# Performance work log

Hardware: AMD Instinct MI355X
Metric: run time of the kernel (lower is better)

The kernel has to match this reference:

```python
import jax, jax.numpy as jnp
import numpy as np

N, E, G = 65536, 262144, 2048
DIN, H, F, L, P, TASK = 9, 300, 32, 5, 3, 1
DG = H + F + 1024 + 167  # 1523


def setup_inputs() -> dict:
    key = jax.random.key(0)
    ks = jax.random.split(key, 24)
    s = 0.02
    inp = {
        'x': jax.random.normal(ks[0], (N, DIN), jnp.float32),
        'morgan': jax.random.uniform(ks[1], (G, 1024), jnp.float32),
        'maccs': jax.random.uniform(ks[2], (G, 167), jnp.float32),
        'edge_index': jax.random.randint(ks[3], (2, E), 0, N, jnp.int32),
        'batch': jnp.sort(jax.random.randint(ks[4], (N,), 0, G, jnp.int32)),
        # node feature encoder
        'W_emb': s * jax.random.normal(ks[5], (DIN, H), jnp.float32),
        'b_emb': jnp.zeros((H,), jnp.float32),
        # GIN conv MLPs (L layers): H -> 2H -> H
        'gin_W1': s * jax.random.normal(ks[6], (L, H, 2 * H), jnp.float32),
        'gin_b1': jnp.zeros((L, 2 * H), jnp.float32),
        'gin_W2': s * jax.random.normal(ks[7], (L, 2 * H, H), jnp.float32),
        'gin_b2': jnp.zeros((L, H), jnp.float32),
        'bn_scale': jnp.ones((L, H), jnp.float32),
        'bn_bias': jnp.zeros((L, H), jnp.float32),
        'eps': jnp.zeros((L,), jnp.float32),
        # virtual node: init embedding + update MLPs (L-1 layers)
        'vn0': jnp.zeros((H,), jnp.float32),
        'vn_W1': s * jax.random.normal(ks[8], (L - 1, H, 2 * H), jnp.float32),
        'vn_b1': jnp.zeros((L - 1, 2 * H), jnp.float32),
        'vn_W2': s * jax.random.normal(ks[9], (L - 1, 2 * H, H), jnp.float32),
        'vn_b2': jnp.zeros((L - 1, H), jnp.float32),
        # predictor MLP: DG -> 2H -> TASK
        'Wp1': s * jax.random.normal(ks[10], (DG, 2 * H), jnp.float32),
        'bp1': jnp.zeros((2 * H,), jnp.float32),
        'Wp2': s * jax.random.normal(ks[11], (2 * H, TASK), jnp.float32),
        'bp2': jnp.zeros((TASK,), jnp.float32),
    }
    return inp


def _seg_mean(v, seg, n):
    s = jax.ops.segment_sum(v, seg, num_segments=n)
    c = jax.ops.segment_sum(jnp.ones((v.shape[0], 1), v.dtype), seg, num_segments=n)
    return s / jnp.maximum(c, 1.0)


def _bn(z, scale, bias):
    m = z.mean(0)
    v = z.var(0)
    return (z - m) * jax.lax.rsqrt(v + 1e-5) * scale + bias


def _gnn_and_predict(x, morgan, maccs, W_emb, b_emb, gin_W1, gin_b1, gin_W2, gin_b2,
                     bn_scale, bn_bias, eps, vn0, vn_W1, vn_b1, vn_W2, vn_b2,
                     Wp1, bp1, Wp2, bp2, edge_index, batch):
    n = x.shape[0]
    g = morgan.shape[0]
    nl = gin_W1.shape[0]
    src, dst = edge_index[0], edge_index[1]

    # GIN-virtual backbone (eval mode, dropout off). Note: GNN input is the
    # original x (the permuted ids are appended AFTER the GNN), so h is
    # permutation-independent and computed once.
    h = x @ W_emb + b_emb
    vn = jnp.broadcast_to(vn0, (g, vn0.shape[0]))
    for l in range(nl):
        hv = h + vn[batch]                                       # [N,H]
        agg = jax.ops.segment_sum(hv[src], dst, num_segments=n)  # neighbor sum
        z = (1.0 + eps[l]) * hv + agg
        z = jax.nn.relu(z @ gin_W1[l] + gin_b1[l]) @ gin_W2[l] + gin_b2[l]
        z = _bn(z, bn_scale[l], bn_bias[l])
        if l < nl - 1:
            z = jax.nn.relu(z)
        h = h + z  # residual
        if l < nl - 1:  # virtual node update
            vt = jax.ops.segment_sum(hv, batch, num_segments=g) + vn
            vn = vn + jax.nn.relu(jax.nn.relu(vt @ vn_W1[l] + vn_b1[l]) @ vn_W2[l] + vn_b2[l])

    pooled_h = _seg_mean(h, batch, g)  # [G,H]

    # Segmented random permutation of tiled eye(F) ids, averaged over P perms.
    # Each node gets one_hot(perm_rank_within_graph % F); rank computed by a
    # single lexsort over (batch, random) instead of a per-graph Python loop.
    counts = jax.ops.segment_sum(jnp.ones((n,), jnp.int32), batch, num_segments=g)
    starts = jnp.concatenate([jnp.zeros((1,), jnp.int32),
                              jnp.cumsum(counts)[:-1].astype(jnp.int32)])
    pkey = jax.random.key(42)
    acc = jnp.zeros((g, F), h.dtype)
    for p in range(P):
        r = jax.random.uniform(jax.random.fold_in(pkey, p), (n,))
        order = jnp.lexsort((r, batch))                       # sort by graph, then random
        local = jnp.arange(n, dtype=jnp.int32) - starts[batch[order]]
        rank = jnp.zeros((n,), jnp.int32).at[order].set(local)  # random rank in graph
        ids = jax.nn.one_hot(rank % F, F, dtype=h.dtype)        # [N,F]
        acc = acc + _seg_mean(ids, batch, g)
    id_pool = acc / P

    # h_rep order matches torch: [pooled h | pooled ids | morgan | maccs]
    h_rep = jnp.concatenate([pooled_h, id_pool, morgan, maccs], axis=1)  # [G,1523]
    return jax.nn.relu(h_rep @ Wp1 + bp1) @ Wp2 + bp2  # [G,TASK]


def reference(x, morgan, maccs, W_emb, b_emb, gin_W1, gin_b1, gin_W2, gin_b2,
              bn_scale, bn_bias, eps, vn0, vn_W1, vn_b1, vn_W2, vn_b2,
              Wp1, bp1, Wp2, bp2, edge_index, batch):
    return _gnn_and_predict(x, morgan, maccs, W_emb, b_emb, gin_W1, gin_b1,
                            gin_W2, gin_b2, bn_scale, bn_bias, eps, vn0,
                            vn_W1, vn_b1, vn_W2, vn_b2, Wp1, bp1, Wp2, bp2,
                            edge_index, batch)
```

## Files before the change

kernel.cpp:

```cpp
#include <hip/hip_runtime.h>

typedef unsigned short u16;
typedef unsigned int u32;
typedef __attribute__((ext_vector_type(8))) short bf16x8_t;
typedef __attribute__((ext_vector_type(4))) float f32x4_t;

#define kN 65536
#define kE 262144
#define kG 2048
#define kH 300
#define kH2 600
#define kL 5
#define kF 32
#define kDG 1523
#define KP_H 320
#define KP_H2 640
#define KP_DG 1536
#define NP_H2 640
#define NP_H 320
#define HVS 320
#define HVS32 160

__device__ __forceinline__ float bf2f(u16 x) {
    union { u32 u; float f; } v; v.u = ((u32)x) << 16; return v.f;
}
__device__ __forceinline__ u16 f2bf(float f) {
    union { float f; u32 u; } v; v.f = f;
    u32 u = v.u;
    u32 r = (u + 0x7fffu + ((u >> 16) & 1u)) >> 16;
    return (u16)r;
}
__device__ __forceinline__ float blo(u32 v) { return bf2f((u16)(v & 0xffffu)); }
__device__ __forceinline__ float bhi(u32 v) { return bf2f((u16)(v >> 16)); }
__device__ __forceinline__ u32 pack2(float lo, float hi) {
    return (u32)f2bf(lo) | ((u32)f2bf(hi) << 16);
}

__device__ __forceinline__ void gld16(const u16* g, u16* l) {
    __builtin_amdgcn_global_load_lds(
        (const __attribute__((address_space(1))) u32*)g,
        (__attribute__((address_space(3))) u32*)l, 16, 0, 0);
}

__device__ __forceinline__ void vwait6() { asm volatile("s_waitcnt vmcnt(6)" ::: "memory"); }
__device__ __forceinline__ void vwait8() { asm volatile("s_waitcnt vmcnt(8)" ::: "memory"); }
__device__ __forceinline__ void vwait0() { asm volatile("s_waitcnt vmcnt(0)" ::: "memory"); }
__device__ __forceinline__ void rbar() {
    __builtin_amdgcn_sched_barrier(0);
    __builtin_amdgcn_s_barrier();
    __builtin_amdgcn_sched_barrier(0);
}

__device__ __forceinline__ void swz_tile(int& m, int& n) {
    int p = blockIdx.x + gridDim.x * blockIdx.y;
    int xcd = p & 7;
    int q = p >> 3;
    int NB = gridDim.y;
    int mb8 = gridDim.x >> 3;
    m = xcd * mb8 + q / NB;
    n = q % NB;
}

__global__ void transpose_k(const float* __restrict__ W, u16* __restrict__ Wt,
                            int K, int NN, int NP, int KP, long total) {
    long idx = (long)blockIdx.x * 256 + threadIdx.x;
    if (idx >= total) return;
    int per = NP * KP;
    int b = (int)(idx / per);
    int r = (int)(idx % per);
    int n = r / KP;
    int k = r % KP;
    u16 v = 0;
    if (n < NN && k < K) v = f2bf(W[(long)b * K * NN + (long)k * NN + n]);
    Wt[idx] = v;
}

__global__ void hist_g_k(const int* __restrict__ batch, int* __restrict__ counts) {
    int n = blockIdx.x * 256 + threadIdx.x;
    if (n < kN) atomicAdd(&counts[batch[n]], 1);
}

__global__ void scan_g_k(const int* __restrict__ counts, int* __restrict__ starts) {
    __shared__ int s[1024];
    int t = threadIdx.x;
    int c0 = counts[2 * t], c1 = counts[2 * t + 1];
    s[t] = c0 + c1;
    __syncthreads();
    for (int off = 1; off < 1024; off <<= 1) {
        int v = (t >= off) ? s[t - off] : 0;
        __syncthreads();
        s[t] += v;
        __syncthreads();
    }
    int excl = (t > 0) ? s[t - 1] : 0;
    starts[2 * t] = excl;
    starts[2 * t + 1] = excl + c0;
}

__global__ void hist_n_k(const int* __restrict__ ei, int* __restrict__ cnt) {
    int e = blockIdx.x * 256 + threadIdx.x;
    if (e < kE) atomicAdd(&cnt[ei[kE + e]], 1);
}

__global__ void scanA_k(const int* __restrict__ cnt, int* __restrict__ start, int* __restrict__ bsum) {
    __shared__ int s[1024];
    int b = blockIdx.x, t = threadIdx.x;
    int v = cnt[b * 1024 + t];
    s[t] = v;
    __syncthreads();
    for (int off = 1; off < 1024; off <<= 1) {
        int u = (t >= off) ? s[t - off] : 0;
        __syncthreads();
        s[t] += u;
        __syncthreads();
    }
    start[b * 1024 + t] = s[t] - v;
    if (t == 1023) bsum[b] = s[1023];
}

__global__ void scanB_k(int* __restrict__ bsum) {
    if (threadIdx.x == 0) {
        int s = 0;
        for (int i = 0; i < kN / 1024; i++) { s += bsum[i]; bsum[i] = s; }
    }
}

__global__ void scanC_k(int* __restrict__ start, const int* __restrict__ bsum) {
    int b = blockIdx.x, t = threadIdx.x;
    int add = (b > 0) ? bsum[b - 1] : 0;
    start[b * 1024 + t] += add;
    if (b == kN / 1024 - 1 && t == 1023) start[kN] = bsum[kN / 1024 - 1];
}

__global__ void fill_n_k(const int* __restrict__ ei, const int* __restrict__ start,
                         int* __restrict__ fill, int* __restrict__ perm) {
    int e = blockIdx.x * 256 + threadIdx.x;
    if (e >= kE) return;
    int s = ei[e], d = ei[kE + e];
    int pos = start[d] + atomicAdd(&fill[d], 1);
    perm[pos] = s;
}

__global__ __launch_bounds__(256) void embed_k(
    const float* __restrict__ x, const float* __restrict__ W,
    const float* __restrict__ b, const float* __restrict__ vn0,
    u32* __restrict__ hv32) {
    __shared__ float sW[9 * kH];
    __shared__ float sBV[kH];
    int tid = threadIdx.x;
    for (int i = tid; i < 9 * kH; i += 256) sW[i] = W[i];
    for (int i = tid; i < kH; i += 256) sBV[i] = b[i] + vn0[i];
    __syncthreads();
    int wave = tid >> 6, lane = tid & 63;
    int n = blockIdx.x * 4 + wave;
    float xv[9];
    #pragma unroll
    for (int d = 0; d < 9; d++) xv[d] = x[n * 9 + d];
    #pragma unroll
    for (int p = 0; p < 3; p++) {
        int ii = lane + p * 64;
        if (ii < 150) {
            int c0 = 2 * ii;
            float a0 = sBV[c0], a1 = sBV[c0 + 1];
            #pragma unroll
            for (int d = 0; d < 9; d++) {
                a0 += xv[d] * sW[d * kH + c0];
                a1 += xv[d] * sW[d * kH + c0 + 1];
            }
            hv32[(long)n * HVS32 + ii] = pack2(a0, a1);
        } else if (ii < HVS32) {
            hv32[(long)n * HVS32 + ii] = 0u;
        }
    }
}

__global__ void vninit_k(const float* __restrict__ vn0, float* __restrict__ vn) {
    int g = blockIdx.x, c = threadIdx.x;
    if (c < kH) vn[g * kH + c] = vn0[c];
}

__global__ __launch_bounds__(256) void gather_combine_k(
    const u32* __restrict__ hv32, const int* __restrict__ start_n,
    const int* __restrict__ perm, const float* __restrict__ eps, int l,
    u32* __restrict__ out32, float* __restrict__ stats) {
    int tid = threadIdx.x;
    int wave = tid >> 6, lane = tid & 63;
    int n = blockIdx.x * 4 + wave;
    int st = start_n[n], en = start_n[n + 1];
    int i0 = lane, i1 = lane + 64, i2 = lane + 128;
    bool p2 = (i2 < 150);
    float a0 = 0.f, b0 = 0.f, a1 = 0.f, b1 = 0.f, a2 = 0.f, b2 = 0.f;
    int e = st;
    for (; e + 4 <= en; e += 4) {
        const u32* rA = hv32 + (long)perm[e] * HVS32;
        const u32* rB = hv32 + (long)perm[e + 1] * HVS32;
        const u32* rC = hv32 + (long)perm[e + 2] * HVS32;
        const u32* rD = hv32 + (long)perm[e + 3] * HVS32;
        u32 vA0 = rA[i0], vA1 = rA[i1], vA2 = p2 ? rA[i2] : 0u;
        u32 vB0 = rB[i0], vB1 = rB[i1], vB2 = p2 ? rB[i2] : 0u;
        u32 vC0 = rC[i0], vC1 = rC[i1], vC2 = p2 ? rC[i2] : 0u;
        u32 vD0 = rD[i0], vD1 = rD[i1], vD2 = p2 ? rD[i2] : 0u;
        a0 += (blo(vA0) + blo(vB0)) + (blo(vC0) + blo(vD0));
        b0 += (bhi(vA0) + bhi(vB0)) + (bhi(vC0) + bhi(vD0));
        a1 += (blo(vA1) + blo(vB1)) + (blo(vC1) + blo(vD1));
        b1 += (bhi(vA1) + bhi(vB1)) + (bhi(vC1) + bhi(vD1));
        a2 += (blo(vA2) + blo(vB2)) + (blo(vC2) + blo(vD2));
        b2 += (bhi(vA2) + bhi(vB2)) + (bhi(vC2) + bhi(vD2));
    }
    for (; e + 2 <= en; e += 2) {
        const u32* rA = hv32 + (long)perm[e] * HVS32;
        const u32* rB = hv32 + (long)perm[e + 1] * HVS32;
        u32 vA0 = rA[i0], vA1 = rA[i1], vA2 = p2 ? rA[i2] : 0u;
        u32 vB0 = rB[i0], vB1 = rB[i1], vB2 = p2 ? rB[i2] : 0u;
        a0 += blo(vA0) + blo(vB0); b0 += bhi(vA0) + bhi(vB0);
        a1 += blo(vA1) + blo(vB1); b1 += bhi(vA1) + bhi(vB1);
        a2 += blo(vA2) + blo(vB2); b2 += bhi(vA2) + bhi(vB2);
    }
    if (e < en) {
        const u32* rA = hv32 + (long)perm[e] * HVS32;
        u32 vA0 = rA[i0], vA1 = rA[i1], vA2 = p2 ? rA[i2] : 0u;
        a0 += blo(vA0); b0 += bhi(vA0);
        a1 += blo(vA1); b1 += bhi(vA1);
        a2 += blo(vA2); b2 += bhi(vA2);
    }
    const u32* self = hv32 + (long)n * HVS32;
    float ep = 1.f + eps[l];
    u32 s0 = self[i0], s1 = self[i1];
    u32* o = out32 + (long)n * HVS32;
    o[i0] = pack2(ep * blo(s0) + a0, ep * bhi(s0) + b0);
    o[i1] = pack2(ep * blo(s1) + a1, ep * bhi(s1) + b1);
    if (p2) {
        u32 s2 = self[i2];
        o[i2] = pack2(ep * blo(s2) + a2, ep * bhi(s2) + b2);
    } else if (i2 < HVS32) {
        o[i2] = 0u;
    }
    int gz = blockIdx.x * 256 + tid;
    if (gz < 2 * kH) stats[gz] = 0.f;
}

__global__ __launch_bounds__(256) void vt_fin_k(
    const u32* __restrict__ hv32, const float* __restrict__ vncur,
    const int* __restrict__ counts, const int* __restrict__ starts,
    u32* __restrict__ vt32) {
    int tid = threadIdx.x, wave = tid >> 6, lane = tid & 63;
    int g = blockIdx.x * 4 + wave;
    int cnt = counts[g], st = starts[g];
    int i0 = lane, i1 = lane + 64, i2 = lane + 128;
    bool p2 = (i2 < 150);
    float a0 = 0.f, b0 = 0.f, a1 = 0.f, b1 = 0.f, a2 = 0.f, b2 = 0.f;
    int i = 0;
    for (; i + 4 <= cnt; i += 4) {
        const u32* rA = hv32 + (long)(st + i) * HVS32;
        const u32* rB = hv32 + (long)(st + i + 1) * HVS32;
        const u32* rC = hv32 + (long)(st + i + 2) * HVS32;
        const u32* rD = hv32 + (long)(st + i + 3) * HVS32;
        u32 vA0 = rA[i0], vA1 = rA[i1], vA2 = p2 ? rA[i2] : 0u;
        u32 vB0 = rB[i0], vB1 = rB[i1], vB2 = p2 ? rB[i2] : 0u;
        u32 vC0 = rC[i0], vC1 = rC[i1], vC2 = p2 ? rC[i2] : 0u;
        u32 vD0 = rD[i0], vD1 = rD[i1], vD2 = p2 ? rD[i2] : 0u;
        a0 += (blo(vA0) + blo(vB0)) + (blo(vC0) + blo(vD0));
        b0 += (bhi(vA0) + bhi(vB0)) + (bhi(vC0) + bhi(vD0));
        a1 += (blo(vA1) + blo(vB1)) + (blo(vC1) + blo(vD1));
        b1 += (bhi(vA1) + bhi(vB1)) + (bhi(vC1) + bhi(vD1));
        a2 += (blo(vA2) + blo(vB2)) + (blo(vC2) + blo(vD2));
        b2 += (bhi(vA2) + bhi(vB2)) + (bhi(vC2) + bhi(vD2));
    }
    for (; i < cnt; i++) {
        const u32* rA = hv32 + (long)(st + i) * HVS32;
        u32 vA0 = rA[i0], vA1 = rA[i1], vA2 = p2 ? rA[i2] : 0u;
        a0 += blo(vA0); b0 += bhi(vA0);
        a1 += blo(vA1); b1 += bhi(vA1);
        a2 += blo(vA2); b2 += bhi(vA2);
    }
    const float* vg = vncur + g * kH;
    vt32[(long)g * HVS32 + i0] = pack2(a0 + vg[2 * i0], b0 + vg[2 * i0 + 1]);
    vt32[(long)g * HVS32 + i1] = pack2(a1 + vg[2 * i1], b1 + vg[2 * i1 + 1]);
    if (p2) vt32[(long)g * HVS32 + i2] = pack2(a2 + vg[2 * i2], b2 + vg[2 * i2 + 1]);
    else if (i2 < HVS32) vt32[(long)g * HVS32 + i2] = 0u;
}

template<int ACT, int OUT_BF16, int BN_STATS>
__global__ __launch_bounds__(256) void gemm_k(
    const u16* __restrict__ A, const u16* __restrict__ Wt,
    const float* __restrict__ bias, void* __restrict__ out,
    float* __restrict__ stats,
    int KP, int NN, int out_stride, int store_cols) {
    __shared__ __align__(16) u16 lA[2][128 * 64];
    __shared__ __align__(16) u16 lB[2][128 * 64];
    __shared__ float sred[128][2];

    const int tid = threadIdx.x;
    const int lane = tid & 63;
    const int wave = tid >> 6;
    const int l16 = lane & 15;
    const int quad = lane >> 4;
    const int wm = (wave & 1) * 64;
    const int wn = (wave >> 1) * 64;
    int sm, sn;
    swz_tile(sm, sn);
    const long tm = (long)sm * 128;
    const int tn = sn * 128;

    const int srow = lane >> 3;
    const int sch = (lane & 7) ^ srow;

    f32x4_t acc[4][4];
    #pragma unroll
    for (int i = 0; i < 4; i++)
        #pragma unroll
        for (int j = 0; j < 4; j++) acc[i][j] = (f32x4_t){0.f, 0.f, 0.f, 0.f};

    auto stage = [&](int bb, int k0) {
        #pragma unroll
        for (int j = 0; j < 4; j++) {
            int rb = wave * 32 + j * 8;
            int r = rb + srow;
            gld16(A + (tm + r) * KP + k0 + sch * 8, &lA[bb][rb * 64]);
            gld16(Wt + (long)(tn + r) * KP + k0 + sch * 8, &lB[bb][rb * 64]);
        }
    };

    const int nk = KP >> 6;
    stage(0, 0);
    if (nk > 1) stage(1, 64);
    for (int t = 0; t < nk; t++) {
        if (t < nk - 1) vwait8(); else vwait0();
        rbar();
        const u16* la = lA[t & 1];
        const u16* lb = lB[t & 1];
        #pragma unroll
        for (int ks = 0; ks < 2; ks++) {
            bf16x8_t af[4], bfr[4];
            #pragma unroll
            for (int mt = 0; mt < 4; mt++) {
                int row = wm + mt * 16 + l16;
                int phys = (ks * 4 + quad) ^ (l16 & 7);
                af[mt] = *(const bf16x8_t*)&la[row * 64 + phys * 8];
            }
            #pragma unroll
            for (int nt = 0; nt < 4; nt++) {
                int row = wn + nt * 16 + l16;
                int phys = (ks * 4 + quad) ^ (l16 & 7);
                bfr[nt] = *(const bf16x8_t*)&lb[row * 64 + phys * 8];
            }
            #pragma unroll
            for (int mt = 0; mt < 4; mt++)
                #pragma unroll
                for (int nt = 0; nt < 4; nt++)
                    acc[mt][nt] = __builtin_amdgcn_mfma_f32_16x16x32_bf16(af[mt], bfr[nt], acc[mt][nt], 0, 0, 0);
        }
        rbar();
        if (t + 2 < nk) stage(t & 1, (t + 2) * 64);
    }

    if (BN_STATS) {
        if (tid < 128) { sred[tid][0] = 0.f; sred[tid][1] = 0.f; }
    }
    __syncthreads();

    #pragma unroll
    for (int nt = 0; nt < 4; nt++) {
        int col = tn + wn + nt * 16 + l16;
        float bv = (col < NN) ? bias[col] : 0.f;
        float s = 0.f, s2 = 0.f;
        #pragma unroll
        for (int mt = 0; mt < 4; mt++) {
            #pragma unroll
            for (int r = 0; r < 4; r++) {
                long row = tm + wm + mt * 16 + quad * 4 + r;
                float v = acc[mt][nt][r] + bv;
                if (ACT) v = fmaxf(v, 0.f);
                float sv = (col < NN) ? v : 0.f;
                if (col < store_cols) {
                    if (OUT_BF16) ((u16*)out)[row * out_stride + col] = f2bf(sv);
                    else          ((float*)out)[row * out_stride + col] = sv;
                }
                s += sv; s2 += sv * sv;
            }
        }
        if (BN_STATS) {
            atomicAdd(&sred[wn + nt * 16 + l16][0], s);
            atomicAdd(&sred[wn + nt * 16 + l16][1], s2);
        }
    }
    if (BN_STATS) {
        __syncthreads();
        if (tid < 128) {
            int col = tn + tid;
            if (col < NN) {
                atomicAdd(&stats[col], sred[tid][0]);
                atomicAdd(&stats[NN + col], sred[tid][1]);
            }
        }
    }
}

template<int ACT, int OUT_MODE, int BN_STATS>
__global__ __launch_bounds__(256) void gemm64_k(
    const u16* __restrict__ A, const u16* __restrict__ Wt,
    const float* __restrict__ bias, void* __restrict__ out,
    float* __restrict__ stats, const float* __restrict__ vnacc,
    int KP, int NN, int out_stride, int store_cols) {
    __shared__ __align__(16) u16 lA[2][128 * 64];
    __shared__ __align__(16) u16 lB[2][64 * 64];
    __shared__ float sred[64][2];

    const int tid = threadIdx.x;
    const int lane = tid & 63;
    const int wave = tid >> 6;
    const int l16 = lane & 15;
    const int quad = lane >> 4;
    const int wm = (wave & 1) * 64;
    const int wn = (wave >> 1) * 32;
    int sm, sn;
    swz_tile(sm, sn);
    const long tm = (long)sm * 128;
    const int tn = sn * 64;

    const int srow = lane >> 3;
    const int sch = (lane & 7) ^ srow;

    f32x4_t acc[4][2];
    #pragma unroll
    for (int i = 0; i < 4; i++)
        #pragma unroll
        for (int j = 0; j < 2; j++) acc[i][j] = (f32x4_t){0.f, 0.f, 0.f, 0.f};

    auto stage = [&](int bb, int k0) {
        #pragma unroll
        for (int j = 0; j < 4; j++) {
            int rb = wave * 32 + j * 8;
            gld16(A + (tm + rb + srow) * KP + k0 + sch * 8, &lA[bb][rb * 64]);
        }
        #pragma unroll
        for (int j = 0; j < 2; j++) {
            int rb = wave * 16 + j * 8;
            gld16(Wt + (long)(tn + rb + srow) * KP + k0 + sch * 8, &lB[bb][rb * 64]);
        }
    };

    const int nk = KP >> 6;
    stage(0, 0);
    if (nk > 1) stage(1, 64);
    for (int t = 0; t < nk; t++) {
        if (t < nk - 1) vwait6(); else vwait0();
        rbar();
        const u16* la = lA[t & 1];
        const u16* lb = lB[t & 1];
        #pragma unroll
        for (int ks = 0; ks < 2; ks++) {
            bf16x8_t af[4], bfr[2];
            #pragma unroll
            for (int mt = 0; mt < 4; mt++) {
                int row = wm + mt * 16 + l16;
                int phys = (ks * 4 + quad) ^ (l16 & 7);
                af[mt] = *(const bf16x8_t*)&la[row * 64 + phys * 8];
            }
            #pragma unroll
            for (int nt = 0; nt < 2; nt++) {
                int row = wn + nt * 16 + l16;
                int phys = (ks * 4 + quad) ^ (l16 & 7);
                bfr[nt] = *(const bf16x8_t*)&lb[row * 64 + phys * 8];
            }
            #pragma unroll
            for (int mt = 0; mt < 4; mt++)
                #pragma unroll
                for (int nt = 0; nt < 2; nt++)
                    acc[mt][nt] = __builtin_amdgcn_mfma_f32_16x16x32_bf16(af[mt], bfr[nt], acc[mt][nt], 0, 0, 0);
        }
        rbar();
        if (t + 2 < nk) stage(t & 1, (t + 2) * 64);
    }

    if (BN_STATS) {
        if (tid < 64) { sred[tid][0] = 0.f; sred[tid][1] = 0.f; }
    }
    __syncthreads();

    #pragma unroll
    for (int nt = 0; nt < 2; nt++) {
        int col = tn + wn + nt * 16 + l16;
        float bv = (col < NN) ? bias[col] : 0.f;
        float s = 0.f, s2 = 0.f;
        #pragma unroll
        for (int mt = 0; mt < 4; mt++) {
            #pragma unroll
            for (int r = 0; r < 4; r++) {
                long row = tm + wm + mt * 16 + quad * 4 + r;
                float v = acc[mt][nt][r] + bv;
                if (ACT) v = fmaxf(v, 0.f);
                float sv = (col < NN) ? v : 0.f;
                if (col < store_cols) {
                    if (OUT_MODE == 1) ((u16*)out)[row * out_stride + col] = f2bf(sv);
                    else if (OUT_MODE == 2)
                        ((float*)out)[row * out_stride + col] =
                            vnacc[row * out_stride + col] + fmaxf(v, 0.f);
                    else ((float*)out)[row * out_stride + col] = sv;
                }
                s += sv; s2 += sv * sv;
            }
        }
        if (BN_STATS) {
            atomicAdd(&sred[wn + nt * 16 + l16][0], s);
            atomicAdd(&sred[wn + nt * 16 + l16][1], s2);
        }
    }
    if (BN_STATS) {
        __syncthreads();
        if (tid < 64) {
            int col = tn + tid;
            if (col < NN) {
                atomicAdd(&stats[col], sred[tid][0]);
                atomicAdd(&stats[NN + col], sred[tid][1]);
            }
        }
    }
}

template<int RELU>
__global__ __launch_bounds__(256) void resid_k(
    u32* __restrict__ hvb32, const u32* __restrict__ z32,
    const float* __restrict__ stats,
    const float* __restrict__ scale, const float* __restrict__ bias, int l,
    const int* __restrict__ batch,
    const float* __restrict__ vncur, const float* __restrict__ vnnxt) {
    int tid = threadIdx.x;
    int wave = tid >> 6, lane = tid & 63;
    int n = blockIdx.x * 4 + wave;
    int g = batch[n];
    #pragma unroll
    for (int p = 0; p < 3; p++) {
        int ii = lane + p * 64;
        if (ii >= 150) break;
        int c0 = 2 * ii;
        float m0 = stats[c0] * (1.f / (float)kN), m1 = stats[c0 + 1] * (1.f / (float)kN);
        float v0 = fmaxf(stats[kH + c0] * (1.f / (float)kN) - m0 * m0, 0.f);
        float v1 = fmaxf(stats[kH + c0 + 1] * (1.f / (float)kN) - m1 * m1, 0.f);
        float a0 = scale[l * kH + c0] * rsqrtf(v0 + 1e-5f);
        float a1 = scale[l * kH + c0 + 1] * rsqrtf(v1 + 1e-5f);
        float d0 = bias[l * kH + c0] - m0 * a0;
        float d1 = bias[l * kH + c0 + 1] - m1 * a1;
        u32 zz = z32[(long)n * HVS32 + ii];
        u32 ho = hvb32[(long)n * HVS32 + ii];
        float2 vc = *(const float2*)(vncur + g * kH + c0);
        float2 vx = *(const float2*)(vnnxt + g * kH + c0);
        float t0 = blo(zz) * a0 + d0;
        float t1 = bhi(zz) * a1 + d1;
        if (RELU) { t0 = fmaxf(t0, 0.f); t1 = fmaxf(t1, 0.f); }
        float h0 = (blo(ho) - vc.x) + t0;
        float h1 = (bhi(ho) - vc.y) + t1;
        hvb32[(long)n * HVS32 + ii] = pack2(h0 + vx.x, h1 + vx.y);
    }
}

__global__ __launch_bounds__(256) void pooled_k(
    const u32* __restrict__ hv32, const float* __restrict__ vnlast,
    const int* __restrict__ counts, const int* __restrict__ starts,
    u32* __restrict__ hrep32) {
    int tid = threadIdx.x, wave = tid >> 6, lane = tid & 63;
    int g = blockIdx.x * 4 + wave;
    int cnt = counts[g], st = starts[g];
    int i0 = lane, i1 = lane + 64, i2 = lane + 128;
    bool p2 = (i2 < 150);
    float a0 = 0.f, b0 = 0.f, a1 = 0.f, b1 = 0.f, a2 = 0.f, b2 = 0.f;
    int i = 0;
    for (; i + 4 <= cnt; i += 4) {
        const u32* rA = hv32 + (long)(st + i) * HVS32;
        const u32* rB = hv32 + (long)(st + i + 1) * HVS32;
        const u32* rC = hv32 + (long)(st + i + 2) * HVS32;
        const u32* rD = hv32 + (long)(st + i + 3) * HVS32;
        u32 vA0 = rA[i0], vA1 = rA[i1], vA2 = p2 ? rA[i2] : 0u;
        u32 vB0 = rB[i0], vB1 = rB[i1], vB2 = p2 ? rB[i2] : 0u;
        u32 vC0 = rC[i0], vC1 = rC[i1], vC2 = p2 ? rC[i2] : 0u;
        u32 vD0 = rD[i0], vD1 = rD[i1], vD2 = p2 ? rD[i2] : 0u;
        a0 += (blo(vA0) + blo(vB0)) + (blo(vC0) + blo(vD0));
        b0 += (bhi(vA0) + bhi(vB0)) + (bhi(vC0) + bhi(vD0));
        a1 += (blo(vA1) + blo(vB1)) + (blo(vC1) + blo(vD1));
        b1 += (bhi(vA1) + bhi(vB1)) + (bhi(vC1) + bhi(vD1));
        a2 += (blo(vA2) + blo(vB2)) + (blo(vC2) + blo(vD2));
        b2 += (bhi(vA2) + bhi(vB2)) + (bhi(vC2) + bhi(vD2));
    }
    for (; i < cnt; i++) {
        const u32* rA = hv32 + (long)(st + i) * HVS32;
        u32 vA0 = rA[i0], vA1 = rA[i1], vA2 = p2 ? rA[i2] : 0u;
        a0 += blo(vA0); b0 += bhi(vA0);
        a1 += blo(vA1); b1 += bhi(vA1);
        a2 += blo(vA2); b2 += bhi(vA2);
    }
    float fc = (float)cnt;
    float inv = 1.f / (float)(cnt > 0 ? cnt : 1);
    const float* vg = vnlast + g * kH;
    hrep32[(long)g * 768 + i0] = pack2((a0 - fc * vg[2 * i0]) * inv, (b0 - fc * vg[2 * i0 + 1]) * inv);
    hrep32[(long)g * 768 + i1] = pack2((a1 - fc * vg[2 * i1]) * inv, (b1 - fc * vg[2 * i1 + 1]) * inv);
    if (p2)
        hrep32[(long)g * 768 + i2] = pack2((a2 - fc * vg[2 * i2]) * inv, (b2 - fc * vg[2 * i2 + 1]) * inv);
}

__global__ void hrep_rest_k(const float* __restrict__ morgan, const float* __restrict__ maccs,
                            const int* __restrict__ counts, u16* __restrict__ hrep) {
    long idx = (long)blockIdx.x * 256 + threadIdx.x;
    if (idx >= (long)kG * (KP_DG - kH)) return;
    int g = (int)(idx / (KP_DG - kH));
    int j = (int)(idx % (KP_DG - kH));
    int col = kH + j;
    u16 v;
    if (j < kF) {
        int c = counts[g];
        int q = (j < c) ? ((c - 1 - j) / kF + 1) : 0;
        v = f2bf((float)q / (float)(c > 0 ? c : 1));
    } else if (j < kF + 1024) {
        v = f2bf(morgan[(long)g * 1024 + (j - kF)]);
    } else if (j < kF + 1024 + 167) {
        v = f2bf(maccs[(long)g * 167 + (j - kF - 1024)]);
    } else {
        v = 0;
    }
    hrep[(long)g * KP_DG + col] = v;
}

__global__ void final_k(const u16* __restrict__ zp, const float* __restrict__ Wp2,
                        const float* __restrict__ bp2, float* __restrict__ out) {
    int wave = threadIdx.x >> 6, lane = threadIdx.x & 63;
    int g = blockIdx.x * 4 + wave;
    float acc = 0.f;
    for (int c = lane; c < kH2; c += 64) acc += bf2f(zp[(long)g * KP_H2 + c]) * Wp2[c];
    #pragma unroll
    for (int off = 32; off; off >>= 1) acc += __shfl_down(acc, off);
    if (lane == 0) out[g] = acc + bp2[0];
}

extern "C" void kernel_launch(void* const* d_in, const int* in_sizes, int n_in,
                              void* d_out, int out_size, void* d_ws, size_t ws_size,
                              hipStream_t stream) {
    const float* x      = (const float*)d_in[0];
    const float* morgan = (const float*)d_in[1];
    const float* maccs  = (const float*)d_in[2];
    const int*   ei     = (const int*)d_in[3];
    const int*   batch  = (const int*)d_in[4];
    const float* W_emb  = (const float*)d_in[5];
    const float* b_emb  = (const float*)d_in[6];
    const float* gin_W1 = (const float*)d_in[7];
    const float* gin_b1 = (const float*)d_in[8];
    const float* gin_W2 = (const float*)d_in[9];
    const float* gin_b2 = (const float*)d_in[10];
    const float* bn_scale = (const float*)d_in[11];
    const float* bn_bias  = (const float*)d_in[12];
    const float* eps    = (const float*)d_in[13];
    const float* vn0    = (const float*)d_in[14];
    const float* vn_W1  = (const float*)d_in[15];
    const float* vn_b1  = (const float*)d_in[16];
    const float* vn_W2  = (const float*)d_in[17];
    const float* vn_b2  = (const float*)d_in[18];
    const float* Wp1    = (const float*)d_in[19];
    const float* bp1    = (const float*)d_in[20];
    const float* Wp2    = (const float*)d_in[21];
    const float* bp2    = (const float*)d_in[22];
    float* out = (float*)d_out;

    char* ws = (char*)d_ws;
    size_t off = 0;
    auto alloc = [&](size_t bytes) -> char* {
        char* p = ws + off;
        off += (bytes + 255) & ~(size_t)255;
        return p;
    };
    u16*   hvbf = (u16*)alloc((size_t)kN * HVS * 2);
    u16*   hv   = (u16*)alloc((size_t)kN * KP_H * 2);
    u16*   z1   = (u16*)alloc((size_t)kN * KP_H2 * 2);
    float* vnA  = (float*)alloc((size_t)kG * kH * 4);
    float* vnB  = (float*)alloc((size_t)kG * kH * 4);
    int* counts = (int*)alloc(kG * 4);
    int* starts = (int*)alloc(kG * 4);
    float* stats = (float*)alloc(2 * kH * 4);
    int* cnt_n  = (int*)alloc((size_t)kN * 4);
    int* start_n = (int*)alloc((size_t)(kN + 1) * 4);
    int* fill_n = (int*)alloc((size_t)kN * 4);
    int* bsum   = (int*)alloc((kN / 1024) * 4);
    int* perm   = (int*)alloc((size_t)kE * 4);
    u16* Wt_g1 = (u16*)alloc((size_t)kL * NP_H2 * KP_H * 2);
    u16* Wt_g2 = (u16*)alloc((size_t)kL * NP_H * KP_H2 * 2);
    u16* Wt_v1 = (u16*)alloc((size_t)(kL - 1) * NP_H2 * KP_H * 2);
    u16* Wt_v2 = (u16*)alloc((size_t)(kL - 1) * NP_H * KP_H2 * 2);
    u16* Wt_p1 = (u16*)alloc((size_t)NP_H2 * KP_DG * 2);
    if (off > ws_size) return;

    u16* vt_in = z1;
    u16* z1v   = z1 + (size_t)4 * 1024 * 1024;
    u16* hrep  = z1;
    u16* zp    = z1 + (size_t)8 * 1024 * 1024;
    float* vnb[2] = {vnA, vnB};

    {
        long t1 = (long)kL * NP_H2 * KP_H;
        transpose_k<<<dim3((unsigned)((t1 + 255) / 256)), 256, 0, stream>>>(gin_W1, Wt_g1, kH, kH2, NP_H2, KP_H, t1);
        long t2 = (long)kL * NP_H * KP_H2;
        transpose_k<<<dim3((unsigned)((t2 + 255) / 256)), 256, 0, stream>>>(gin_W2, Wt_g2, kH2, kH, NP_H, KP_H2, t2);
        long t3 = (long)(kL - 1) * NP_H2 * KP_H;
        transpose_k<<<dim3((unsigned)((t3 + 255) / 256)), 256, 0, stream>>>(vn_W1, Wt_v1, kH, kH2, NP_H2, KP_H, t3);
        long t4 = (long)(kL - 1) * NP_H * KP_H2;
        transpose_k<<<dim3((unsigned)((t4 + 255) / 256)), 256, 0, stream>>>(vn_W2, Wt_v2, kH2, kH, NP_H, KP_H2, t4);
        long t5 = (long)NP_H2 * KP_DG;
        transpose_k<<<dim3((unsigned)((t5 + 255) / 256)), 256, 0, stream>>>(Wp1, Wt_p1, kDG, kH2, NP_H2, KP_DG, t5);
    }

    hipMemsetAsync(counts, 0, kG * 4, stream);
    hipMemsetAsync(cnt_n, 0, (size_t)kN * 4, stream);
    hipMemsetAsync(fill_n, 0, (size_t)kN * 4, stream);
    hist_g_k<<<kN / 256, 256, 0, stream>>>(batch, counts);
    scan_g_k<<<1, 1024, 0, stream>>>(counts, starts);
    hist_n_k<<<kE / 256, 256, 0, stream>>>(ei, cnt_n);
    scanA_k<<<kN / 1024, 1024, 0, stream>>>(cnt_n, start_n, bsum);
    scanB_k<<<1, 64, 0, stream>>>(bsum);
    scanC_k<<<kN / 1024, 1024, 0, stream>>>(start_n, bsum);
    fill_n_k<<<kE / 256, 256, 0, stream>>>(ei, start_n, fill_n, perm);

    embed_k<<<kN / 4, 256, 0, stream>>>(x, W_emb, b_emb, vn0, (u32*)hvbf);
    vninit_k<<<kG, 320, 0, stream>>>(vn0, vnA);

    for (int l = 0; l < kL; l++) {
        float* vcur = vnb[l & 1];
        float* vnxt = vnb[(l + 1) & 1];
        gather_combine_k<<<kN / 4, 256, 0, stream>>>(
            (const u32*)hvbf, start_n, perm, eps, l, (u32*)hv, stats);
        if (l < kL - 1) {
            vt_fin_k<<<kG / 4, 256, 0, stream>>>(
                (const u32*)hvbf, vcur, counts, starts, (u32*)vt_in);
            gemm_k<1, 1, 0><<<dim3(16, NP_H2 / 128), 256, 0, stream>>>(
                vt_in, Wt_v1 + (size_t)l * NP_H2 * KP_H, vn_b1 + l * kH2,
                z1v, nullptr, KP_H, kH2, KP_H2, KP_H2);
            gemm64_k<0, 2, 0><<<dim3(16, NP_H / 64), 256, 0, stream>>>(
                z1v, Wt_v2 + (size_t)l * NP_H * KP_H2, vn_b2 + l * kH,
                vnxt, nullptr, vcur, KP_H2, kH, kH, kH);
        }
        gemm_k<1, 1, 0><<<dim3(kN / 128, NP_H2 / 128), 256, 0, stream>>>(
            hv, Wt_g1 + (size_t)l * NP_H2 * KP_H, gin_b1 + l * kH2,
            z1, nullptr, KP_H, kH2, KP_H2, KP_H2);
        gemm64_k<0, 1, 1><<<dim3(kN / 128, NP_H / 64), 256, 0, stream>>>(
            z1, Wt_g2 + (size_t)l * NP_H * KP_H2, gin_b2 + l * kH,
            hv, stats, nullptr, KP_H2, kH, KP_H, KP_H);
        if (l < kL - 1)
            resid_k<1><<<kN / 4, 256, 0, stream>>>(
                (u32*)hvbf, (const u32*)hv, stats, bn_scale, bn_bias, l, batch, vcur, vnxt);
        else
            resid_k<0><<<kN / 4, 256, 0, stream>>>(
                (u32*)hvbf, (const u32*)hv, stats, bn_scale, bn_bias, l, batch, vcur, vcur);
    }

    float* vnlast = vnb[(kL - 1) & 1];
    pooled_k<<<kG / 4, 256, 0, stream>>>(
        (const u32*)hvbf, vnlast, counts, starts, (u32*)hrep);
    {
        long tr = (long)kG * (KP_DG - kH);
        hrep_rest_k<<<dim3((unsigned)((tr + 255) / 256)), 256, 0, stream>>>(morgan, maccs, counts, hrep);
    }
    gemm_k<1, 1, 0><<<dim3(16, NP_H2 / 128), 256, 0, stream>>>(
        hrep, Wt_p1, bp1, zp, nullptr, KP_DG, kH2, KP_H2, KP_H2);
    final_k<<<kG / 4, 256, 0, stream>>>(zp, Wp2, bp2, out);
}
```

Before: 1.323 ms.

## Fuse GIN two-layer MLP GEMMs into one kernel with z1 kept in LDS

Replaces the separate H→2H and 2H→H GEMM launches in each GIN layer with one 512-thread kernel. Each block computes 128-wide chunks of the hidden activation, applies bias and ReLU, stores the chunk as bf16 in shared memory, and feeds it straight into the second GEMM. The block then writes the output along with BatchNorm statistics. This removes the global write and re-read of the large N×640 intermediate and one launch per layer. In exchange it uses a large shared-memory footprint, which limits occupancy, and it does not double-buffer the W2 tile loads, so stalls may go up.

```diff
diff --git a/kernel.cpp b/kernel.cpp
--- a/kernel.cpp
+++ b/kernel.cpp
@@ -42,6 +42,7 @@
         (__attribute__((address_space(3))) u32*)l, 16, 0, 0);
 }
 
+__device__ __forceinline__ void vwait4() { asm volatile("s_waitcnt vmcnt(4)" ::: "memory"); }
 __device__ __forceinline__ void vwait6() { asm volatile("s_waitcnt vmcnt(6)" ::: "memory"); }
 __device__ __forceinline__ void vwait8() { asm volatile("s_waitcnt vmcnt(8)" ::: "memory"); }
 __device__ __forceinline__ void vwait0() { asm volatile("s_waitcnt vmcnt(0)" ::: "memory"); }
@@ -280,6 +281,187 @@
     else if (i2 < HVS32) vt32[(long)g * HVS32 + i2] = 0u;
 }
 
+__global__ __launch_bounds__(512, 2) void fused_mlp_k(
+    const u16* __restrict__ A,
+    const u16* __restrict__ W1t,
+    const float* __restrict__ b1,
+    const u16* __restrict__ W2t,
+    const float* __restrict__ b2,
+    u16* __restrict__ outp,
+    float* __restrict__ stats) {
+    __shared__ __align__(16) u16 lA[2][128 * 64];
+    __shared__ __align__(16) u16 lW1[2][128 * 64];
+    __shared__ __align__(16) u16 z1c[128 * 128];
+    __shared__ __align__(16) u16 lW2[320 * 64];
+    __shared__ float sred[320][2];
+
+    const int tid = threadIdx.x;
+    const int lane = tid & 63;
+    const int wave = tid >> 6;
+    const int l16 = lane & 15;
+    const int quad = lane >> 4;
+    const long tm = (long)blockIdx.x * 128;
+    const int srow = lane >> 3;
+    const int sch = (lane & 7) ^ srow;
+
+    const int wm = (wave & 1) * 64;
+    const int wnA = (wave >> 1) * 32;
+    const int wnB = (wave >> 1) * 80;
+
+    if (tid < 320) { sred[tid][0] = 0.f; sred[tid][1] = 0.f; }
+
+    float rb1[5][2];
+    #pragma unroll
+    for (int c = 0; c < 5; c++)
+        #pragma unroll
+        for (int nt = 0; nt < 2; nt++) {
+            int gc = c * 128 + wnA + nt * 16 + l16;
+            rb1[c][nt] = (gc < kH2) ? b1[gc] : 0.f;
+        }
+    float rb2[5];
+    #pragma unroll
+    for (int nt = 0; nt < 5; nt++) {
+        int col = wnB + nt * 16 + l16;
+        rb2[nt] = (col < kH) ? b2[col] : 0.f;
+    }
+
+    f32x4_t acc2[4][5];
+    #pragma unroll
+    for (int i = 0; i < 4; i++)
+        #pragma unroll
+        for (int j = 0; j < 5; j++) acc2[i][j] = (f32x4_t){0.f, 0.f, 0.f, 0.f};
+
+    for (int c = 0; c < 5; c++) {
+        f32x4_t acc1[4][2];
+        #pragma unroll
+        for (int i = 0; i < 4; i++) {
+            acc1[i][0] = (f32x4_t){0.f, 0.f, 0.f, 0.f};
+            acc1[i][1] = (f32x4_t){0.f, 0.f, 0.f, 0.f};
+        }
+        auto stageA = [&](int bb, int k0) {
+            #pragma unroll
+            for (int j = 0; j < 2; j++) {
+                int rb = wave * 16 + j * 8;
+                gld16(A + (tm + rb + srow) * KP_H + k0 + sch * 8, &lA[bb][rb * 64]);
+                gld16(W1t + (long)(c * 128 + rb + srow) * KP_H + k0 + sch * 8, &lW1[bb][rb * 64]);
+            }
+        };
+        stageA(0, 0);
+        stageA(1, 64);
+        for (int t = 0; t < 5; t++) {
+            if (t < 4) vwait4(); else vwait0();
+            rbar();
+            const u16* la = lA[t & 1];
+            const u16* lw = lW1[t & 1];
+            #pragma unroll
+            for (int ks = 0; ks < 2; ks++) {
+                bf16x8_t af[4], bfr[2];
+                #pragma unroll
+                for (int mt = 0; mt < 4; mt++) {
+                    int row = wm + mt * 16 + l16;
+                    int phys = (ks * 4 + quad) ^ (l16 & 7);
+                    af[mt] = *(const bf16x8_t*)&la[row * 64 + phys * 8];
+                }
+                #pragma unroll
+                for (int nt = 0; nt < 2; nt++) {
+                    int row = wnA + nt * 16 + l16;
+                    int phys = (ks * 4 + quad) ^ (l16 & 7);
+                    bfr[nt] = *(const bf16x8_t*)&lw[row * 64 + phys * 8];
+                }
+                #pragma unroll
+                for (int mt = 0; mt < 4; mt++)
+                    #pragma unroll
+                    for (int nt = 0; nt < 2; nt++)
+                        acc1[mt][nt] = __builtin_amdgcn_mfma_f32_16x16x32_bf16(af[mt], bfr[nt], acc1[mt][nt], 0, 0, 0);
+            }
+            rbar();
+            if (t + 2 < 5) stageA(t & 1, (t + 2) * 64);
+        }
+
+        #pragma unroll
+        for (int j = 0; j < 5; j++) {
+            int rb = wave * 40 + j * 8;
+            gld16(W2t + (long)(rb + srow) * KP_H2 + c * 128 + sch * 8, &lW2[rb * 64]);
+        }
+
+        #pragma unroll
+        for (int nt = 0; nt < 2; nt++) {
+            int col = wnA + nt * 16 + l16;
+            #pragma unroll
+            for (int mt = 0; mt < 4; mt++) {
+                #pragma unroll
+                for (int r = 0; r < 4; r++) {
+                    int row = wm + mt * 16 + quad * 4 + r;
+                    float v = acc1[mt][nt][r] + rb1[c][nt];
+                    v = fmaxf(v, 0.f);
+                    int phys = (col >> 3) ^ (row & 15);
+                    z1c[row * 128 + phys * 8 + (col & 7)] = f2bf(v);
+                }
+            }
+        }
+        __syncthreads();
+
+        #pragma unroll
+        for (int s = 0; s < 2; s++) {
+            #pragma unroll
+            for (int ks = 0; ks < 2; ks++) {
+                bf16x8_t af[4], bfr[5];
+                #pragma unroll
+                for (int mt = 0; mt < 4; mt++) {
+                    int row = wm + mt * 16 + l16;
+                    int phys = (s * 8 + ks * 4 + quad) ^ (row & 15);
+                    af[mt] = *(const bf16x8_t*)&z1c[row * 128 + phys * 8];
+                }
+                #pragma unroll
+                for (int nt = 0; nt < 5; nt++) {
+                    int row = wnB + nt * 16 + l16;
+                    int phys = (ks * 4 + quad) ^ (l16 & 7);
+                    bfr[nt] = *(const bf16x8_t*)&lW2[row * 64 + phys * 8];
+                }
+                #pragma unroll
+                for (int mt = 0; mt < 4; mt++)
+                    #pragma unroll
+                    for (int nt = 0; nt < 5; nt++)
+                        acc2[mt][nt] = __builtin_amdgcn_mfma_f32_16x16x32_bf16(af[mt], bfr[nt], acc2[mt][nt], 0, 0, 0);
+            }
+            rbar();
+            if (s == 0) {
+                #pragma unroll
+                for (int j = 0; j < 5; j++) {
+                    int rb = wave * 40 + j * 8;
+                    gld16(W2t + (long)(rb + srow) * KP_H2 + c * 128 + 64 + sch * 8, &lW2[rb * 64]);
+                }
+                vwait0();
+                rbar();
+            }
+        }
+    }
+
+    #pragma unroll
+    for (int nt = 0; nt < 5; nt++) {
+        int col = wnB + nt * 16 + l16;
+        float s = 0.f, s2 = 0.f;
+        #pragma unroll
+        for (int mt = 0; mt < 4; mt++) {
+            #pragma unroll
+            for (int r = 0; r < 4; r++) {
+                long row = tm + wm + mt * 16 + quad * 4 + r;
+                float v = acc2[mt][nt][r] + rb2[nt];
+                float sv = (col < kH) ? v : 0.f;
+                outp[row * KP_H + col] = f2bf(sv);
+                s += sv; s2 += sv * sv;
+            }
+        }
+        atomicAdd(&sred[col][0], s);
+        atomicAdd(&sred[col][1], s2);
+    }
+    __syncthreads();
+    if (tid < kH) {
+        atomicAdd(&stats[tid], sred[tid][0]);
+        atomicAdd(&stats[kH + tid], sred[tid][1]);
+    }
+}
+
 template<int ACT, int OUT_BF16, int BN_STATS>
 __global__ __launch_bounds__(256) void gemm_k(
     const u16* __restrict__ A, const u16* __restrict__ Wt,
@@ -733,12 +915,10 @@
                 z1v, Wt_v2 + (size_t)l * NP_H * KP_H2, vn_b2 + l * kH,
                 vnxt, nullptr, vcur, KP_H2, kH, kH, kH);
         }
-        gemm_k<1, 1, 0><<<dim3(kN / 128, NP_H2 / 128), 256, 0, stream>>>(
+        fused_mlp_k<<<kN / 128, 512, 0, stream>>>(
             hv, Wt_g1 + (size_t)l * NP_H2 * KP_H, gin_b1 + l * kH2,
-            z1, nullptr, KP_H, kH2, KP_H2, KP_H2);
-        gemm64_k<0, 1, 1><<<dim3(kN / 128, NP_H / 64), 256, 0, stream>>>(
-            z1, Wt_g2 + (size_t)l * NP_H * KP_H2, gin_b2 + l * kH,
-            hv, stats, nullptr, KP_H2, kH, KP_H, KP_H);
+            Wt_g2 + (size_t)l * NP_H * KP_H2, gin_b2 + l * kH,
+            hv, stats);
         if (l < kL - 1)
             resid_k<1><<<kN / 4, 256, 0, stream>>>(
                 (u32*)hvbf, (const u32*)hv, stats, bn_scale, bn_bias, l, batch, vcur, vnxt);
```

After: 1.309 ms. Within noise of the previous version (-1.1%).
